# Kernel optimization log

Measured on AMD Instinct MI355X. Metric: run time of the kernel, lower is better.

The kernel has to match this reference:

```python
import jax, jax.numpy as jnp
import numpy as np
from jax import lax

TOP_K = 8
EPS = 1e-12


def l2_normalize(x, axis):
    sq = jnp.sum(x * x, axis=axis, keepdims=True)
    return x * lax.rsqrt(jnp.maximum(sq, EPS))


def setup_inputs() -> dict:
    key = jax.random.key(0)
    k1, k2, k3, k4 = jax.random.split(key, 4)
    B, N, C = 256, 197, 768
    POOL, LEN = 1024, 8
    x_embed = jax.random.normal(k1, (B, N, C), dtype=jnp.float32)
    prompt = jax.random.uniform(k2, (POOL, LEN, C), dtype=jnp.float32, minval=-1.0, maxval=1.0)
    prompt_key = jax.random.uniform(k3, (POOL, C), dtype=jnp.float32, minval=-1.0, maxval=1.0)
    # kaiming_normal fan_out: std = sqrt(2 / fan_out)
    proj_w = jax.random.normal(k4, (C, C), dtype=jnp.float32) * np.sqrt(2.0 / C).astype(np.float32)
    proj_b = jnp.zeros((C,), dtype=jnp.float32)
    return {"x_embed": x_embed, "prompt": prompt, "prompt_key": prompt_key,
            "proj_w": proj_w, "proj_b": proj_b}


def reference(x_embed, prompt, prompt_key, proj_w, proj_b):
    B = x_embed.shape[0]
    # embedding_key == 'mean'
    x_mean = jnp.mean(x_embed, axis=1)                     # [B, C]
    prompt_norm = l2_normalize(prompt_key, axis=1)         # [P, C]
    x_norm = l2_normalize(x_mean, axis=1)                  # [B, C]
    similarity = x_norm @ prompt_norm.T                    # [B, P]
    _, idx = lax.top_k(similarity, TOP_K)                  # [B, K]
    # gather prompts: [B, K, L, C] -> [B, K*L, C]
    bp = prompt[idx]
    Bk, K, L, C = bp.shape
    batched_prompt = bp.reshape(Bk, K * L, C)
    # projection + residual (dropout in eval mode = identity)
    batched_prompt = batched_prompt @ proj_w.T + proj_b + batched_prompt
    # key loss term
    batched_key_norm = prompt_norm[idx]                    # [B, K, C]
    reduce_sim = jnp.sum(batched_key_norm * x_norm[:, None, :]) / B
    prompted = jnp.concatenate([x_embed[:, :1, :], batched_prompt, x_embed[:, 1:, :]], axis=1)
    return prompted, reduce_sim
```

## Files before the change

### kernel.cpp

```cpp
#include <hip/hip_runtime.h>
#include <float.h>
#include <math.h>

#define B_    256
#define N_    197
#define C_    768
#define POOL_ 1024
#define LEN_  8
#define TOPK_ 8
#define PROWS (POOL_*LEN_)
#define OUTROWS 261

typedef __attribute__((ext_vector_type(8))) short short8_t;
typedef __attribute__((ext_vector_type(4))) float f32x4;

static const size_t OFF_XMEAN = 0;
static const size_t OFF_INVX  = 786432;
static const size_t OFF_INVP  = 787456;
static const size_t OFF_SIM   = 791552;
static const size_t OFF_ACC   = 1840128;
static const size_t OFF_ABF   = 1840384;
static const size_t OFF_WBF   = 14423296;
static const size_t OFF_PROJ  = 15602944;

__device__ __forceinline__ unsigned short f2bf(float f) {
    unsigned int u = __float_as_uint(f);
    u += 0x7fffu + ((u >> 16) & 1u);
    return (unsigned short)(u >> 16);
}

__global__ __launch_bounds__(768) void kA(const float* __restrict__ x,
                                          const float* __restrict__ pkey,
                                          const float* __restrict__ prompt,
                                          const float* __restrict__ projw,
                                          float* __restrict__ out,
                                          float* __restrict__ xmean,
                                          float* __restrict__ invx,
                                          float* __restrict__ invp,
                                          unsigned short* __restrict__ Abf,
                                          unsigned short* __restrict__ Wbf,
                                          float* __restrict__ accum) {
    __shared__ f32x4 red[4][192];
    __shared__ float sq[256];
    __shared__ float wsum[12];
    const int bid = blockIdx.x, t = threadIdx.x;

    if (bid < B_) {
        const int b = bid;
        const int r = t / 192;
        const int c = t - r * 192;
        const f32x4* xin  = (const f32x4*)x   + (size_t)b * (N_ * 192) + c;
        f32x4*       outb = (f32x4*)out       + (size_t)b * (OUTROWS * 192) + c;
        float sx = 0.f, sy = 0.f, sz = 0.f, sw = 0.f;
        #pragma unroll 7
        for (int n = r; n < 196; n += 4) {
            f32x4 v = __builtin_nontemporal_load(&xin[(size_t)n * 192]);
            sx += v.x; sy += v.y; sz += v.z; sw += v.w;
            int orow = (n == 0) ? 0 : (64 + n);
            __builtin_nontemporal_store(v, &outb[(size_t)orow * 192]);
        }
        if (r == 0) {
            f32x4 v = __builtin_nontemporal_load(&xin[(size_t)196 * 192]);
            sx += v.x; sy += v.y; sz += v.z; sw += v.w;
            __builtin_nontemporal_store(v, &outb[(size_t)260 * 192]);
        }
        f32x4 s; s.x = sx; s.y = sy; s.z = sz; s.w = sw;
        red[r][c] = s;
        if (t < 256) sq[t] = 0.f;
        __syncthreads();
        if (r == 0) {
            f32x4 a = red[0][c], b2 = red[1][c], c2 = red[2][c], d = red[3][c];
            const float inv = 1.0f / (float)N_;
            f32x4 m;
            m.x = (a.x + b2.x + c2.x + d.x) * inv;
            m.y = (a.y + b2.y + c2.y + d.y) * inv;
            m.z = (a.z + b2.z + c2.z + d.z) * inv;
            m.w = (a.w + b2.w + c2.w + d.w) * inv;
            ((f32x4*)xmean)[b * 192 + c] = m;
            sq[c] = m.x*m.x + m.y*m.y + m.z*m.z + m.w*m.w;
        }
        __syncthreads();
        for (int off = 128; off > 0; off >>= 1) {
            if (t < off) sq[t] += sq[t + off];
            __syncthreads();
        }
        if (t == 0) {
            invx[b] = 1.0f / sqrtf(fmaxf(sq[0], 1e-12f));
            if (b == 0) { accum[0] = 0.0f; ((int*)accum)[1] = 0; }
        }
    } else if (bid < B_ + POOL_) {
        const int p = bid - B_;
        float v = pkey[(size_t)p * C_ + t];
        float sg = v * v;
        #pragma unroll
        for (int off = 32; off > 0; off >>= 1) sg += __shfl_down(sg, off);
        const int wave = t >> 6;
        if ((t & 63) == 0) wsum[wave] = sg;
        __syncthreads();
        if (t == 0) {
            float tot = wsum[0];
            #pragma unroll
            for (int w = 1; w < 12; ++w) tot += wsum[w];
            invp[p] = 1.0f / sqrtf(fmaxf(tot, 1e-12f));
        }
    } else {
        int i4 = (bid - (B_ + POOL_)) * 768 + t;
        float4 v; unsigned short* d;
        if (i4 < (PROWS * C_ / 4)) {
            v = ((const float4*)prompt)[i4];
            d = Abf + (size_t)i4 * 4;
        } else {
            int j4 = i4 - PROWS * C_ / 4;
            v = ((const float4*)projw)[j4];
            d = Wbf + (size_t)j4 * 4;
        }
        ushort4 o; o.x = f2bf(v.x); o.y = f2bf(v.y); o.z = f2bf(v.z); o.w = f2bf(v.w);
        *(ushort4*)d = o;
    }
}

__global__ __launch_bounds__(256) void kB(const unsigned short* __restrict__ A,
                                          const unsigned short* __restrict__ W,
                                          const float* __restrict__ bias,
                                          const float* __restrict__ resid,
                                          float* __restrict__ projout,
                                          const float* __restrict__ xmean,
                                          const float* __restrict__ pkey,
                                          const float* __restrict__ invx,
                                          const float* __restrict__ invp,
                                          float* __restrict__ sim) {
    __shared__ short As5[2][64*32];
    __shared__ short Bs5[2][128*32];
    __shared__ float As3[32][36];
    __shared__ float Bs3[32][36];
    const int tid = threadIdx.x;
    const int bid = blockIdx.x;

    if (bid < 768) {
        const int m0 = (bid / 6) * 64, n0 = (bid % 6) * 128;
        const int wave = tid >> 6, lane = tid & 63;
        const int quad = lane >> 4, lr = lane & 15;
        const int srow = tid >> 2;
        const int scol = (tid & 3) * 8;

        f32x4 acc[4][2] = {};

        auto stage = [&](int buf, int kt) {
            const int k0 = kt * 32;
            __builtin_amdgcn_global_load_lds(
                (const __attribute__((address_space(1))) void*)&A[(size_t)(m0 + srow) * C_ + k0 + scol],
                (__attribute__((address_space(3))) void*)&As5[buf][srow*32 + scol], 16, 0, 0);
            __builtin_amdgcn_global_load_lds(
                (const __attribute__((address_space(1))) void*)&W[(size_t)(n0 + srow) * C_ + k0 + scol],
                (__attribute__((address_space(3))) void*)&Bs5[buf][srow*32 + scol], 16, 0, 0);
            __builtin_amdgcn_global_load_lds(
                (const __attribute__((address_space(1))) void*)&W[(size_t)(n0 + 64 + srow) * C_ + k0 + scol],
                (__attribute__((address_space(3))) void*)&Bs5[buf][(64 + srow)*32 + scol], 16, 0, 0);
        };
        auto compute = [&](int buf) {
            short8_t af[4], bf[2];
            #pragma unroll
            for (int i = 0; i < 4; ++i)
                af[i] = *(const short8_t*)&As5[buf][(i*16 + lr)*32 + quad*8];
            #pragma unroll
            for (int j = 0; j < 2; ++j)
                bf[j] = *(const short8_t*)&Bs5[buf][(wave*32 + j*16 + lr)*32 + quad*8];
            #pragma unroll
            for (int i = 0; i < 4; ++i)
                #pragma unroll
                for (int j = 0; j < 2; ++j)
                    acc[i][j] = __builtin_amdgcn_mfma_f32_16x16x32_bf16(af[i], bf[j], acc[i][j], 0, 0, 0);
        };

        stage(0, 0);
        __syncthreads();
        int cur = 0;
        for (int kt = 0; kt < 23; ++kt) {
            stage(cur ^ 1, kt + 1);
            compute(cur);
            __syncthreads();
            cur ^= 1;
        }
        compute(cur);

        #pragma unroll
        for (int j = 0; j < 2; ++j) {
            const int n = n0 + wave*32 + j*16 + lr;
            const float bn = bias[n];
            #pragma unroll
            for (int i = 0; i < 4; ++i) {
                const int mbase = m0 + i*16 + quad*4;
                #pragma unroll
                for (int r = 0; r < 4; ++r) {
                    const int m = mbase + r;
                    projout[(size_t)m * C_ + n] = acc[i][j][r] + bn + resid[(size_t)m * C_ + n];
                }
            }
        }
    } else {
        const int q = bid - 768;
        const int m0 = (q >> 5) * 32, n0 = (q & 31) * 32;
        const int t = tid;
        const int lrow = t >> 3, lc = (t & 7) * 4;
        const int ty = t >> 4, tx = t & 15;
        float a00 = 0.f, a01 = 0.f, a10 = 0.f, a11 = 0.f;
        float4 va = *(const float4*)&xmean[(size_t)(m0 + lrow) * C_ + lc];
        float4 vb = *(const float4*)&pkey [(size_t)(n0 + lrow) * C_ + lc];
        for (int k0 = 0; k0 < C_; k0 += 32) {
            __syncthreads();
            *(float4*)&As3[lrow][lc] = va;
            *(float4*)&Bs3[lrow][lc] = vb;
            __syncthreads();
            if (k0 + 32 < C_) {
                va = *(const float4*)&xmean[(size_t)(m0 + lrow) * C_ + k0 + 32 + lc];
                vb = *(const float4*)&pkey [(size_t)(n0 + lrow) * C_ + k0 + 32 + lc];
            }
            #pragma unroll
            for (int kk = 0; kk < 32; kk += 4) {
                float4 A0 = *(const float4*)&As3[ty*2][kk];
                float4 A1 = *(const float4*)&As3[ty*2+1][kk];
                float4 B0 = *(const float4*)&Bs3[tx*2][kk];
                float4 B1 = *(const float4*)&Bs3[tx*2+1][kk];
                a00 += A0.x*B0.x; a00 += A0.y*B0.y; a00 += A0.z*B0.z; a00 += A0.w*B0.w;
                a01 += A0.x*B1.x; a01 += A0.y*B1.y; a01 += A0.z*B1.z; a01 += A0.w*B1.w;
                a10 += A1.x*B0.x; a10 += A1.y*B0.y; a10 += A1.z*B0.z; a10 += A1.w*B0.w;
                a11 += A1.x*B1.x; a11 += A1.y*B1.y; a11 += A1.z*B1.z; a11 += A1.w*B1.w;
            }
        }
        const float im0 = invx[m0 + ty*2], im1 = invx[m0 + ty*2 + 1];
        const float ip0 = invp[n0 + tx*2], ip1 = invp[n0 + tx*2 + 1];
        sim[(size_t)(m0 + ty*2    ) * POOL_ + n0 + tx*2    ] = a00 * im0 * ip0;
        sim[(size_t)(m0 + ty*2    ) * POOL_ + n0 + tx*2 + 1] = a01 * im0 * ip1;
        sim[(size_t)(m0 + ty*2 + 1) * POOL_ + n0 + tx*2    ] = a10 * im1 * ip0;
        sim[(size_t)(m0 + ty*2 + 1) * POOL_ + n0 + tx*2 + 1] = a11 * im1 * ip1;
    }
}

__global__ __launch_bounds__(256) void kC(const float* __restrict__ sim,
                                          const float* __restrict__ projall,
                                          float* __restrict__ accum,
                                          float* __restrict__ out) {
    __shared__ float vals[POOL_];
    __shared__ float wv[4];
    __shared__ int   wi[4];
    __shared__ int   sidx[TOPK_];
    const int b = blockIdx.x, t = threadIdx.x;
    const int wave = t >> 6, lane = t & 63;
    #pragma unroll
    for (int i = 0; i < 4; ++i) vals[t + 256*i] = sim[(size_t)b * POOL_ + t + 256*i];
    __syncthreads();
    float sumv = 0.0f;
    for (int k = 0; k < TOPK_; ++k) {
        float bv = -FLT_MAX; int bi = POOL_;
        #pragma unroll
        for (int i = 0; i < 4; ++i) {
            int n = t + 256*i;
            float v = vals[n];
            if (v > bv) { bv = v; bi = n; }
        }
        #pragma unroll
        for (int off = 32; off > 0; off >>= 1) {
            float v2 = __shfl_down(bv, off);
            int   i2 = __shfl_down(bi, off);
            if (v2 > bv || (v2 == bv && i2 < bi)) { bv = v2; bi = i2; }
        }
        if (lane == 0) { wv[wave] = bv; wi[wave] = bi; }
        __syncthreads();
        if (t == 0) {
            float fv = wv[0]; int fi = wi[0];
            #pragma unroll
            for (int w = 1; w < 4; ++w) {
                float v2 = wv[w]; int i2 = wi[w];
                if (v2 > fv || (v2 == fv && i2 < fi)) { fv = v2; fi = i2; }
            }
            sidx[k] = fi;
            sumv += fv;
            vals[fi] = -FLT_MAX;
        }
        __syncthreads();
    }
    #pragma unroll 4
    for (int jj = 0; jj < 16; ++jj) {
        const int j = wave * 16 + jj;
        const int p = sidx[j >> 3];
        const int l = j & 7;
        const f32x4* src = (const f32x4*)projall + (size_t)(p * LEN_ + l) * 192;
        f32x4* dst = (f32x4*)out + (size_t)(b * OUTROWS + 1 + j) * 192;
        __builtin_nontemporal_store(src[lane],       &dst[lane]);
        __builtin_nontemporal_store(src[lane + 64],  &dst[lane + 64]);
        __builtin_nontemporal_store(src[lane + 128], &dst[lane + 128]);
    }
    if (t == 0) {
        atomicAdd(&accum[0], sumv);
        __threadfence();
        int done = atomicAdd((int*)accum + 1, 1);
        if (done == B_ - 1) {
            float tot = atomicAdd(&accum[0], 0.0f);
            out[(size_t)B_ * OUTROWS * C_] = tot * (1.0f / (float)B_);
        }
    }
}

extern "C" void kernel_launch(void* const* d_in, const int* in_sizes, int n_in,
                              void* d_out, int out_size, void* d_ws, size_t ws_size,
                              hipStream_t stream) {
    const float* x_embed = (const float*)d_in[0];
    const float* prompt  = (const float*)d_in[1];
    const float* pkey    = (const float*)d_in[2];
    const float* projw   = (const float*)d_in[3];
    const float* projb   = (const float*)d_in[4];
    float* out = (float*)d_out;
    char* ws = (char*)d_ws;

    float*          xmean   = (float*)(ws + OFF_XMEAN);
    float*          invx    = (float*)(ws + OFF_INVX);
    float*          invp    = (float*)(ws + OFF_INVP);
    float*          sim     = (float*)(ws + OFF_SIM);
    float*          acc     = (float*)(ws + OFF_ACC);
    unsigned short* Abf     = (unsigned short*)(ws + OFF_ABF);
    unsigned short* Wbf     = (unsigned short*)(ws + OFF_WBF);
    float*          projall = (float*)(ws + OFF_PROJ);

    const int convBlocks = (PROWS * C_ / 4 + 768 * 768 / 4) / 768;
    kA<<<B_ + POOL_ + convBlocks, 768, 0, stream>>>(x_embed, pkey, prompt, projw,
                                                    out, xmean, invx, invp, Abf, Wbf, acc);
    kB<<<1024, 256, 0, stream>>>(Abf, Wbf, projb, prompt, projall,
                                 xmean, pkey, invx, invp, sim);
    kC<<<B_, 256, 0, stream>>>(sim, projall, acc, out);
}
```

Baseline: 423.8 us.

## Fuse L2-norm computation into similarity GEMM and shrink kA blocks to 256 threads

Stops computing the inverse norms of x_mean and prompt_key in separate blocks of the first kernel. Each similarity tile now accumulates its own row sums of squares while staging data and normalizes locally. The first kernel is re-split into 256-thread blocks, three per batch row for the mean/copy and finer blocks for the bf16 conversion. The aim is to remove the extra pkey pass and the 1024 norm blocks and to raise occupancy, at the cost of redundant norm work across similarity tiles and a shared-memory union in kB.

```diff
diff --git a/kernel.cpp b/kernel.cpp
--- a/kernel.cpp
+++ b/kernel.cpp
@@ -15,13 +15,11 @@
 typedef __attribute__((ext_vector_type(4))) float f32x4;
 
 static const size_t OFF_XMEAN = 0;
-static const size_t OFF_INVX  = 786432;
-static const size_t OFF_INVP  = 787456;
-static const size_t OFF_SIM   = 791552;
-static const size_t OFF_ACC   = 1840128;
-static const size_t OFF_ABF   = 1840384;
-static const size_t OFF_WBF   = 14423296;
-static const size_t OFF_PROJ  = 15602944;
+static const size_t OFF_SIM   = 786432;
+static const size_t OFF_ACC   = 1835008;
+static const size_t OFF_ABF   = 1835264;
+static const size_t OFF_WBF   = 14418176;
+static const size_t OFF_PROJ  = 15597824;
 
 __device__ __forceinline__ unsigned short f2bf(float f) {
     unsigned int u = __float_as_uint(f);
@@ -29,28 +27,24 @@
     return (unsigned short)(u >> 16);
 }
 
-__global__ __launch_bounds__(768) void kA(const float* __restrict__ x,
-                                          const float* __restrict__ pkey,
+__global__ __launch_bounds__(256) void kA(const float* __restrict__ x,
                                           const float* __restrict__ prompt,
                                           const float* __restrict__ projw,
                                           float* __restrict__ out,
                                           float* __restrict__ xmean,
-                                          float* __restrict__ invx,
-                                          float* __restrict__ invp,
                                           unsigned short* __restrict__ Abf,
                                           unsigned short* __restrict__ Wbf,
                                           float* __restrict__ accum) {
-    __shared__ f32x4 red[4][192];
-    __shared__ float sq[256];
-    __shared__ float wsum[12];
     const int bid = blockIdx.x, t = threadIdx.x;
-
-    if (bid < B_) {
-        const int b = bid;
-        const int r = t / 192;
-        const int c = t - r * 192;
-        const f32x4* xin  = (const f32x4*)x   + (size_t)b * (N_ * 192) + c;
-        f32x4*       outb = (f32x4*)out       + (size_t)b * (OUTROWS * 192) + c;
+    if (bid == 0 && t == 0) { accum[0] = 0.0f; ((int*)accum)[1] = 0; }
+    if (bid < B_ * 3) {
+        __shared__ f32x4 red[4][64];
+        const int b = bid / 3, seg = bid % 3;
+        const int r = t >> 6;
+        const int c = t & 63;
+        const int c4 = seg * 64 + c;
+        const f32x4* xin  = (const f32x4*)x   + (size_t)b * (N_ * 192) + c4;
+        f32x4*       outb = (f32x4*)out       + (size_t)b * (OUTROWS * 192) + c4;
         float sx = 0.f, sy = 0.f, sz = 0.f, sw = 0.f;
         #pragma unroll 7
         for (int n = r; n < 196; n += 4) {
@@ -66,7 +60,6 @@
         }
         f32x4 s; s.x = sx; s.y = sy; s.z = sz; s.w = sw;
         red[r][c] = s;
-        if (t < 256) sq[t] = 0.f;
         __syncthreads();
         if (r == 0) {
             f32x4 a = red[0][c], b2 = red[1][c], c2 = red[2][c], d = red[3][c];
@@ -76,35 +69,10 @@
             m.y = (a.y + b2.y + c2.y + d.y) * inv;
             m.z = (a.z + b2.z + c2.z + d.z) * inv;
             m.w = (a.w + b2.w + c2.w + d.w) * inv;
-            ((f32x4*)xmean)[b * 192 + c] = m;
-            sq[c] = m.x*m.x + m.y*m.y + m.z*m.z + m.w*m.w;
-        }
-        __syncthreads();
-        for (int off = 128; off > 0; off >>= 1) {
-            if (t < off) sq[t] += sq[t + off];
-            __syncthreads();
-        }
-        if (t == 0) {
-            invx[b] = 1.0f / sqrtf(fmaxf(sq[0], 1e-12f));
-            if (b == 0) { accum[0] = 0.0f; ((int*)accum)[1] = 0; }
-        }
-    } else if (bid < B_ + POOL_) {
-        const int p = bid - B_;
-        float v = pkey[(size_t)p * C_ + t];
-        float sg = v * v;
-        #pragma unroll
-        for (int off = 32; off > 0; off >>= 1) sg += __shfl_down(sg, off);
-        const int wave = t >> 6;
-        if ((t & 63) == 0) wsum[wave] = sg;
-        __syncthreads();
-        if (t == 0) {
-            float tot = wsum[0];
-            #pragma unroll
-            for (int w = 1; w < 12; ++w) tot += wsum[w];
-            invp[p] = 1.0f / sqrtf(fmaxf(tot, 1e-12f));
+            ((f32x4*)xmean)[b * 192 + c4] = m;
         }
     } else {
-        int i4 = (bid - (B_ + POOL_)) * 768 + t;
+        int i4 = (bid - B_ * 3) * 256 + t;
         float4 v; unsigned short* d;
         if (i4 < (PROWS * C_ / 4)) {
             v = ((const float4*)prompt)[i4];
@@ -126,17 +94,14 @@
                                           float* __restrict__ projout,
                                           const float* __restrict__ xmean,
                                           const float* __restrict__ pkey,
-                                          const float* __restrict__ invx,
-                                          const float* __restrict__ invp,
                                           float* __restrict__ sim) {
-    __shared__ short As5[2][64*32];
-    __shared__ short Bs5[2][128*32];
-    __shared__ float As3[32][36];
-    __shared__ float Bs3[32][36];
+    __shared__ __align__(16) char smem[24576];
     const int tid = threadIdx.x;
     const int bid = blockIdx.x;
 
     if (bid < 768) {
+        short (*As5)[64*32]  = (short (*)[64*32])(smem);
+        short (*Bs5)[128*32] = (short (*)[128*32])(smem + 8192);
         const int m0 = (bid / 6) * 64, n0 = (bid % 6) * 128;
         const int wave = tid >> 6, lane = tid & 63;
         const int quad = lane >> 4, lr = lane & 15;
@@ -198,18 +163,26 @@
             }
         }
     } else {
+        float (*As3)[36] = (float (*)[36])(smem);
+        float (*Bs3)[36] = (float (*)[36])(smem + 4608);
+        float* sqA  = (float*)(smem + 9216);
+        float* sqB  = (float*)(smem + 10240);
+        float* invs = (float*)(smem + 11264);
         const int q = bid - 768;
         const int m0 = (q >> 5) * 32, n0 = (q & 31) * 32;
         const int t = tid;
         const int lrow = t >> 3, lc = (t & 7) * 4;
         const int ty = t >> 4, tx = t & 15;
         float a00 = 0.f, a01 = 0.f, a10 = 0.f, a11 = 0.f;
+        float sqa = 0.f, sqb = 0.f;
         float4 va = *(const float4*)&xmean[(size_t)(m0 + lrow) * C_ + lc];
         float4 vb = *(const float4*)&pkey [(size_t)(n0 + lrow) * C_ + lc];
         for (int k0 = 0; k0 < C_; k0 += 32) {
             __syncthreads();
             *(float4*)&As3[lrow][lc] = va;
             *(float4*)&Bs3[lrow][lc] = vb;
+            sqa += va.x*va.x + va.y*va.y + va.z*va.z + va.w*va.w;
+            sqb += vb.x*vb.x + vb.y*vb.y + vb.z*vb.z + vb.w*vb.w;
             __syncthreads();
             if (k0 + 32 < C_) {
                 va = *(const float4*)&xmean[(size_t)(m0 + lrow) * C_ + k0 + 32 + lc];
@@ -227,8 +200,20 @@
                 a11 += A1.x*B1.x; a11 += A1.y*B1.y; a11 += A1.z*B1.z; a11 += A1.w*B1.w;
             }
         }
-        const float im0 = invx[m0 + ty*2], im1 = invx[m0 + ty*2 + 1];
-        const float ip0 = invp[n0 + tx*2], ip1 = invp[n0 + tx*2 + 1];
+        sqA[lrow*8 + (t & 7)] = sqa;
+        sqB[lrow*8 + (t & 7)] = sqb;
+        __syncthreads();
+        if (t < 64) {
+            const float* s = (t < 32) ? sqA : sqB;
+            const int rr = t & 31;
+            float tot = 0.f;
+            #pragma unroll
+            for (int j = 0; j < 8; ++j) tot += s[rr*8 + j];
+            invs[t] = 1.0f / sqrtf(fmaxf(tot, 1e-12f));
+        }
+        __syncthreads();
+        const float im0 = invs[ty*2], im1 = invs[ty*2 + 1];
+        const float ip0 = invs[32 + tx*2], ip1 = invs[32 + tx*2 + 1];
         sim[(size_t)(m0 + ty*2    ) * POOL_ + n0 + tx*2    ] = a00 * im0 * ip0;
         sim[(size_t)(m0 + ty*2    ) * POOL_ + n0 + tx*2 + 1] = a01 * im0 * ip1;
         sim[(size_t)(m0 + ty*2 + 1) * POOL_ + n0 + tx*2    ] = a10 * im1 * ip0;
@@ -313,18 +298,16 @@
     char* ws = (char*)d_ws;
 
     float*          xmean   = (float*)(ws + OFF_XMEAN);
-    float*          invx    = (float*)(ws + OFF_INVX);
-    float*          invp    = (float*)(ws + OFF_INVP);
     float*          sim     = (float*)(ws + OFF_SIM);
     float*          acc     = (float*)(ws + OFF_ACC);
     unsigned short* Abf     = (unsigned short*)(ws + OFF_ABF);
     unsigned short* Wbf     = (unsigned short*)(ws + OFF_WBF);
     float*          projall = (float*)(ws + OFF_PROJ);
 
-    const int convBlocks = (PROWS * C_ / 4 + 768 * 768 / 4) / 768;
-    kA<<<B_ + POOL_ + convBlocks, 768, 0, stream>>>(x_embed, pkey, prompt, projw,
-                                                    out, xmean, invx, invp, Abf, Wbf, acc);
+    const int convBlocks = (PROWS * C_ / 4 + 768 * 768 / 4) / 256;
+    kA<<<B_ * 3 + convBlocks, 256, 0, stream>>>(x_embed, prompt, projw,
+                                                out, xmean, Abf, Wbf, acc);
     kB<<<1024, 256, 0, stream>>>(Abf, Wbf, projb, prompt, projall,
-                                 xmean, pkey, invx, invp, sim);
+                                 xmean, pkey, sim);
     kC<<<B_, 256, 0, stream>>>(sim, projall, acc, out);
 }
```

Result: no change. 421.9 us (-0.4%).
